# Performance work log

Measured on AMD Instinct MI355X. Metric: run time of the kernel, lower is better.

Reference implementation:

```python
import jax, jax.numpy as jnp
import numpy as np

B, N, K, NC, EMB, Z, AD = 16, 2048, 20, 16, 1024, 256, 64

def _lrelu(x):
    return jnp.where(x > 0, x, 0.2 * x)

def _bn(x, g, b, axes):
    # BatchNorm (training-mode batch stats, biased var, eps=1e-5); channel axis = 1
    m = x.mean(axes, keepdims=True)
    v = x.var(axes, keepdims=True)
    sh = [1] * x.ndim; sh[1] = -1
    return (x - m) * jax.lax.rsqrt(v + 1e-5) * g.reshape(sh) + b.reshape(sh)

def _c2(w, x):  # 1x1 Conv2d, no bias
    return jnp.einsum('oc,bcnk->bonk', w, x)

def _c1(w, x):  # 1x1 Conv1d, no bias
    return jnp.einsum('oc,bcn->bon', w, x)

def _knn(x, k):  # x: (B,C,N) -> idx (B,N,k)
    inner = -2.0 * jnp.einsum('bcn,bcm->bnm', x, x)
    xx = jnp.sum(x * x, axis=1)  # (B,N)
    pd = -xx[:, :, None] - inner - xx[:, None, :]  # negative squared dist
    return jax.lax.top_k(pd, k)[1]

def _graph_feat(x, idx):  # x: (B,C,N), idx: (B,N,k) -> (B,2C,N,k)
    xt = x.transpose(0, 2, 1)  # (B,N,C)
    feat = jax.vmap(lambda a, i: a[i])(xt, idx)  # (B,N,k,C)
    xc = jnp.broadcast_to(xt[:, :, None, :], feat.shape)
    return jnp.concatenate([feat - xc, xc], axis=-1).transpose(0, 3, 1, 2)

def setup_inputs():
    key = jax.random.key(0)
    ks = jax.random.split(key, 16)
    rn = lambda k, sh: (jax.random.normal(k, sh) * 0.05).astype(jnp.float32)
    d = {
        'xyz': jax.random.normal(ks[0], (B, N, 3), jnp.float32),
        'flow': jax.random.normal(ks[1], (B, N, 3), jnp.float32),
        'eps': jax.random.normal(ks[2], (B, Z), jnp.float32),
        'w_c1a': rn(ks[3], (60, 6)),   'w_c1b': rn(ks[4], (60, 60)),
        'w_c2a': rn(ks[5], (60, 120)), 'w_c2b': rn(ks[6], (60, 60)),
        'w_c3': rn(ks[7], (EMB, 120)),
        'w_mu': rn(ks[8], (Z, EMB)),  'b_mu': jnp.zeros((Z,), jnp.float32),
        'w_var': rn(ks[9], (Z, EMB)), 'b_var': jnp.zeros((Z,), jnp.float32),
        'w_enc': rn(ks[10], (64, NC)),
        'w_cub1': rn(ks[11], (256, Z + 64)), 'w_cub2': rn(ks[12], (120, 256)),
        'w_q': rn(ks[13], (AD, 120)), 'w_k': rn(ks[14], (AD, 120)),
    }
    for nm, c in [('c1a', 60), ('c1b', 60), ('c2a', 60), ('c2b', 60), ('c3', EMB)]:
        d['g_' + nm] = jnp.ones((c,), jnp.float32)
        d['bb_' + nm] = jnp.zeros((c,), jnp.float32)
    return d

def reference(xyz, flow, eps, w_c1a, w_c1b, w_c2a, w_c2b, w_c3, w_mu, b_mu,
              w_var, b_var, w_enc, w_cub1, w_cub2, w_q, w_k,
              g_c1a, bb_c1a, g_c1b, bb_c1b, g_c2a, bb_c2a, g_c2b, bb_c2b, g_c3, bb_c3):
    x = xyz.transpose(0, 2, 1)  # (B,3,N)
    idx = _knn(x, K)
    h = _graph_feat(x, idx)  # (B,6,N,K)
    h = _lrelu(_bn(_c2(w_c1a, h), g_c1a, bb_c1a, (0, 2, 3)))
    h = _lrelu(_bn(_c2(w_c1b, h), g_c1b, bb_c1b, (0, 2, 3)))
    x1 = h.max(axis=-1)  # (B,60,N)
    h = _graph_feat(x1, idx)  # low_dim_idx=1: reuse xyz knn
    h = _lrelu(_bn(_c2(w_c2a, h), g_c2a, bb_c2a, (0, 2, 3)))
    h = _lrelu(_bn(_c2(w_c2b, h), g_c2b, bb_c2b, (0, 2, 3)))
    x2 = h.max(axis=-1)
    x_per = jnp.concatenate([x1, x2], axis=1)  # (B,120,N)
    g = _lrelu(_bn(_c1(w_c3, x_per), g_c3, bb_c3, (0, 2))).max(axis=-1)  # (B,EMB)
    mu = g @ w_mu.T + b_mu
    log_var = g @ w_var.T + b_var
    z = eps * jnp.exp(0.5 * log_var) + mu  # (B,Z)
    cub = jnp.broadcast_to(jnp.eye(NC, dtype=xyz.dtype), (xyz.shape[0], NC, NC))
    cvec = _lrelu(_c1(w_enc, cub))  # (B,64,NC)
    xc = jnp.concatenate([jnp.broadcast_to(z[:, :, None], (z.shape[0], Z, NC)), cvec], axis=1)
    xc = _lrelu(_c1(w_cub1, xc))
    x_cuboid = _lrelu(_c1(w_cub2, xc))  # (B,120,NC)
    Q = _c1(w_q, x_per) / jnp.sqrt(jnp.float32(AD))  # (B,AD,N)
    Kf = _c1(w_k, x_cuboid)  # (B,AD,NC)
    scores = jnp.einsum('bcm,bcn->bmn', Kf, Q)  # (B,NC,N)
    assign = jax.nn.softmax(scores, axis=1).transpose(0, 2, 1)  # (B,N,NC)
    return (x_per, x_cuboid, z[:, :, None], mu, log_var, assign)
```

## Files before the change

kernel.cpp:

```cpp
#include <hip/hip_runtime.h>

typedef unsigned int u32;
typedef unsigned short u16;

#define BB 16
#define NN 2048
#define KK 20
#define EE (BB*NN*KK)
#define PP (BB*NN)
#define NCHK 8
#define CHKSZ (NN/NCHK)

#define O_XPER 0
#define O_XCUB 3932160
#define O_Z    3962880
#define O_MU   3966976
#define O_LV   3971072
#define O_ASG  3975168

__device__ double g_part[524288];
__device__ double g_std[2560];
__device__ float  g_st[2560];
__device__ float  g_zf[BB*256];
__device__ float  g_Kf[BB*1024];
__device__ u16    g_idx[EE];
__device__ float  g_xpf[(size_t)PP*120];
__device__ float  g_e1[(size_t)EE*60];
__device__ float  g_e2[(size_t)EE*60];

#define S1B_D 128
#define S2A_D 256
#define S2B_D 384
#define S1A_AB 0
#define S1B_AB 128
#define S2A_AB 256
#define S2B_AB 384
#define S3A 512
#define S3B 1536

#define MB_OFF 320000

#define NEG_BIG -1.0e30f

__device__ __forceinline__ float lrelu(float x){ return x > 0.f ? x : 0.2f*x; }

__device__ __forceinline__ void xrow(int bn, int c0, int cnt, float* d){
  const float* s = g_xpf + (size_t)bn*120 + c0;
  #pragma unroll 4
  for (int i=0;i<cnt;i+=4){
    float4 v = *(const float4*)(s+i);
    d[i]=v.x; d[i+1]=v.y; d[i+2]=v.z; d[i+3]=v.w;
  }
}

__device__ __forceinline__ float pdcalc(float4 pm, float qx, float qy, float qz, float qw){
  float dot = fmaf(qx,pm.x, fmaf(qy,pm.y, qz*pm.z));
  float t = fmaf(2.f, dot, -qw);
  return t - pm.w;
}

#define KT_DECL \
  float td0=NEG_BIG,td1=NEG_BIG,td2=NEG_BIG,td3=NEG_BIG,td4=NEG_BIG, \
        td5=NEG_BIG,td6=NEG_BIG,td7=NEG_BIG,td8=NEG_BIG,td9=NEG_BIG, \
        td10=NEG_BIG,td11=NEG_BIG,td12=NEG_BIG,td13=NEG_BIG,td14=NEG_BIG, \
        td15=NEG_BIG,td16=NEG_BIG,td17=NEG_BIG,td18=NEG_BIG,td19=NEG_BIG;
#define KT_CSW(u,l) { float mx = fmaxf(td##u, td##l); float mn = fminf(td##u, td##l); td##u = mx; td##l = mn; }
#define KT_INSERT(pd) \
  if ((pd) > td19){ \
    td19 = (pd); \
    KT_CSW(18,19) KT_CSW(17,18) KT_CSW(16,17) KT_CSW(15,16) \
    KT_CSW(14,15) KT_CSW(13,14) KT_CSW(12,13) KT_CSW(11,12) \
    KT_CSW(10,11) KT_CSW(9,10)  KT_CSW(8,9)   KT_CSW(7,8)   \
    KT_CSW(6,7)   KT_CSW(5,6)   KT_CSW(4,5)   KT_CSW(3,4)   \
    KT_CSW(2,3)   KT_CSW(1,2)   KT_CSW(0,1) }

__global__ __launch_bounds__(128) void k_knnt(const float* __restrict__ xyz){
  __shared__ float4 cand[CHKSZ];
  int qg = blockIdx.x >> 3;
  int c  = blockIdx.x & 7;
  int b  = qg >> 4;
  int n0 = (qg & 15) << 7;
  int t  = threadIdx.x;
  int m0 = c*CHKSZ;
  for (int i=t;i<CHKSZ;i+=128){
    const float* s = xyz + ((size_t)((b<<11)+m0+i))*3;
    float x=s[0], y=s[1], z=s[2];
    cand[i] = make_float4(x,y,z, fmaf(x,x,fmaf(y,y,z*z)));
  }
  __syncthreads();
  int n = n0 + t;
  const float* qs = xyz + ((size_t)((b<<11)+n))*3;
  float qx=qs[0], qy=qs[1], qz=qs[2];
  float qw = fmaf(qx,qx,fmaf(qy,qy,qz*qz));
  KT_DECL
  for (int i=0;i<CHKSZ;i++){
    float pd = pdcalc(cand[i], qx,qy,qz,qw);
    KT_INSERT(pd)
  }
  int p = (b<<11) + n;
  float* outd = g_e1;
  #define KOUT(k) outd[(size_t)(c*KK+k)*PP + p] = td##k;
  KOUT(0) KOUT(1) KOUT(2) KOUT(3) KOUT(4) KOUT(5) KOUT(6) KOUT(7) KOUT(8) KOUT(9)
  KOUT(10) KOUT(11) KOUT(12) KOUT(13) KOUT(14) KOUT(15) KOUT(16) KOUT(17) KOUT(18) KOUT(19)
  #undef KOUT
}

__global__ __launch_bounds__(256) void k_knnu(){
  int q = blockIdx.x*256 + threadIdx.x;
  const float* ind = g_e1;
  KT_DECL
  for (int i=0;i<NCHK*KK;i++){
    float pd = ind[(size_t)i*PP + q];
    KT_INSERT(pd)
  }
  g_e2[q] = td19;
}

__global__ __launch_bounds__(256) void k_knns1(const float* __restrict__ xyz){
  __shared__ float4 cand[CHKSZ];
  int gid = blockIdx.x*256 + threadIdx.x;
  int c = gid >> 15;
  int q = gid & (PP-1);
  int b = q >> 11;
  int t = threadIdx.x;
  for (int i=t;i<CHKSZ;i+=256){
    const float* s = xyz + ((size_t)((b<<11)+c*CHKSZ+i))*3;
    float x=s[0], y=s[1], z=s[2];
    cand[i] = make_float4(x,y,z, fmaf(x,x,fmaf(y,y,z*z)));
  }
  __syncthreads();
  const float* qs = xyz + (size_t)q*3;
  float qx=qs[0], qy=qs[1], qz=qs[2];
  float qw = fmaf(qx,qx,fmaf(qy,qy,qz*qz));
  float T = g_e2[q];
  u32 cgt=0, ceq=0;
  for (int i=0;i<CHKSZ;i++){
    float pd = pdcalc(cand[i], qx,qy,qz,qw);
    cgt += (pd > T) ? 1u : 0u;
    ceq += (pd == T) ? 1u : 0u;
  }
  u32* cntg = (u32*)g_part;
  u32* cnte = cntg + NCHK*PP;
  cntg[c*PP + q] = cgt;
  cnte[c*PP + q] = ceq;
}

__global__ __launch_bounds__(256) void k_knns2(){
  int q = blockIdx.x*256 + threadIdx.x;
  u32* cntg = (u32*)g_part;
  u32* cnte = cntg + NCHK*PP;
  u32* bg   = cnte + NCHK*PP;
  u32* be   = bg   + NCHK*PP;
  u32 acc = 0;
  for (int c=0;c<NCHK;c++){ bg[c*PP+q] = acc; acc += cntg[c*PP+q]; }
  u32 eacc = acc;
  for (int c=0;c<NCHK;c++){ be[c*PP+q] = eacc; eacc += cnte[c*PP+q]; }
}

__global__ __launch_bounds__(256) void k_knns3(const float* __restrict__ xyz){
  __shared__ float4 cand[CHKSZ];
  int gid = blockIdx.x*256 + threadIdx.x;
  int c = gid >> 15;
  int q = gid & (PP-1);
  int b = q >> 11;
  int t = threadIdx.x;
  for (int i=t;i<CHKSZ;i+=256){
    const float* s = xyz + ((size_t)((b<<11)+c*CHKSZ+i))*3;
    float x=s[0], y=s[1], z=s[2];
    cand[i] = make_float4(x,y,z, fmaf(x,x,fmaf(y,y,z*z)));
  }
  __syncthreads();
  const float* qs = xyz + (size_t)q*3;
  float qx=qs[0], qy=qs[1], qz=qs[2];
  float qw = fmaf(qx,qx,fmaf(qy,qy,qz*qz));
  float T = g_e2[q];
  const u32* cntg = (const u32*)g_part;
  const u32* cnte = cntg + NCHK*PP;
  const u32* bg   = cnte + NCHK*PP;
  const u32* be   = bg   + NCHK*PP;
  u32 wgt = bg[c*PP+q];
  u32 weq = be[c*PP+q];
  u16* o = g_idx + (size_t)q*KK;
  for (int i=0;i<CHKSZ;i++){
    float pd = pdcalc(cand[i], qx,qy,qz,qw);
    int m = c*CHKSZ + i;
    if (pd > T && wgt < KK){ o[wgt] = (u16)m; wgt++; }
    else if (pd == T && weq < KK){ o[weq] = (u16)m; weq++; }
  }
}

__global__ __launch_bounds__(256) void k_red60(int dbase, int nblk){
  __shared__ double red[256];
  int s = blockIdx.x;
  int t = threadIdx.x;
  double acc = 0.0;
  for (int i=t;i<nblk;i+=256) acc += g_part[(size_t)i*128 + s];
  red[t] = acc; __syncthreads();
  for (int w=128; w>0; w>>=1){ if (t<w) red[t]+=red[t+w]; __syncthreads(); }
  if (t==0) g_std[dbase+s] = red[0];
}

__global__ __launch_bounds__(64) void k_fin(const float* __restrict__ g, const float* __restrict__ bb,
                                            int dbase, int abase, double invc){
  int c = threadIdx.x;
  if (c < 60){
    double m = g_std[dbase+c]*invc;
    double v = g_std[dbase+64+c]*invc - m*m;
    if (v < 0.0) v = 0.0;
    float r = (float)(1.0/sqrt(v + 1e-5));
    float a = r*g[c];
    g_st[abase+c] = a;
    g_st[abase+64+c] = bb[c] - (float)m*a;
  }
}

__global__ __launch_bounds__(256) void k_gram1(const float* __restrict__ xyz){
  __shared__ double sred[128];
  int tid = threadIdx.x, lane = tid & 63, wv = tid >> 6;
  double acc[27];
  #pragma unroll
  for (int k=0;k<27;k++) acc[k]=0.0;
  for (int it=0; it<8; ++it){
    int edge = (it*320 + blockIdx.x)*256 + tid;
    int row = edge / KK;
    int b = row >> 11;
    int nbr = g_idx[edge];
    const float* cp = xyz + (size_t)row*3;
    const float* np2 = xyz + ((size_t)((b<<11)+nbr))*3;
    float f3=cp[0], f4=cp[1], f5=cp[2];
    float f0=np2[0]-f3, f1=np2[1]-f4, f2=np2[2]-f5;
    float f[6] = {f0,f1,f2,f3,f4,f5};
    #pragma unroll
    for (int i=0;i<6;i++) acc[i] += (double)f[i];
    int k=6;
    #pragma unroll
    for (int i=0;i<6;i++)
      #pragma unroll
      for (int j=i;j<6;j++){ acc[k] += (double)f[i]*(double)f[j]; k++; }
  }
  #pragma unroll
  for (int k=0;k<27;k++){
    double s = acc[k];
    #pragma unroll
    for (int m=1;m<64;m<<=1) s += __shfl_xor(s,m);
    if (lane==0) sred[wv*32+k] = s;
  }
  __syncthreads();
  if (tid < 27)
    g_part[(size_t)blockIdx.x*32 + tid] = sred[tid] + sred[32+tid] + sred[64+tid] + sred[96+tid];
}

__global__ __launch_bounds__(64) void k_fing1(const float* __restrict__ w1a,
                                              const float* __restrict__ gg, const float* __restrict__ bb){
  __shared__ double gsum[27];
  int t = threadIdx.x;
  if (t < 27){
    double s = 0.0;
    for (int i=0;i<320;i++) s += g_part[(size_t)i*32 + t];
    gsum[t] = s;
  }
  __syncthreads();
  if (t < 60){
    float w[6];
    #pragma unroll
    for (int i=0;i<6;i++) w[i] = w1a[t*6+i];
    double S = 0.0;
    #pragma unroll
    for (int i=0;i<6;i++) S += (double)w[i]*gsum[i];
    double Q = 0.0; int k = 6;
    #pragma unroll
    for (int i=0;i<6;i++)
      #pragma unroll
      for (int j=i;j<6;j++){
        double cf = (i==j) ? 1.0 : 2.0;
        Q += cf*(double)w[i]*(double)w[j]*gsum[k]; k++;
      }
    double inv1 = 1.0/(double)EE;
    double m = S*inv1;
    double v = Q*inv1 - m*m;
    if (v < 0.0) v = 0.0;
    float r = (float)(1.0/sqrt(v + 1e-5));
    float A = r*gg[t];
    g_st[S1A_AB+t] = A;
    g_st[S1A_AB+64+t] = bb[t] - (float)m*A;
  }
}

__global__ __launch_bounds__(256) void k_conv1b(const float* __restrict__ xyz,
                                                const float* __restrict__ w1a, const float* __restrict__ w1b){
  __shared__ float ws[360];
  __shared__ float wbs[3600];
  __shared__ float As[60], Bs[60];
  __shared__ double sred[512];
  int tid = threadIdx.x, lane = tid & 63, wv = tid >> 6;
  for (int i=tid;i<360;i+=256) ws[i]=w1a[i];
  for (int i=tid;i<3600;i+=256) wbs[i]=w1b[i];
  if (tid<60){ As[tid]=g_st[S1A_AB+tid]; Bs[tid]=g_st[S1A_AB+64+tid]; }
  __syncthreads();
  int edge = blockIdx.x*256 + tid;
  int row = edge / KK;
  int b = row >> 11;
  int nbr = g_idx[edge];
  const float* cp = xyz + (size_t)row*3;
  const float* np2 = xyz + ((size_t)((b<<11)+nbr))*3;
  float c0=cp[0], c1=cp[1], c2=cp[2];
  float d0=np2[0]-c0, d1=np2[1]-c1, d2=np2[2]-c2;
  float h[60];
  #pragma unroll 4
  for (int o=0;o<60;o++){
    float y = ws[o*6]*d0 + ws[o*6+1]*d1 + ws[o*6+2]*d2 + ws[o*6+3]*c0 + ws[o*6+4]*c1 + ws[o*6+5]*c2;
    h[o] = lrelu(fmaf(As[o], y, Bs[o]));
  }
  double rs=0.0, rq=0.0;
  for (int o=0;o<60;o++){
    float y=0.f;
    #pragma unroll
    for (int c=0;c<60;c++) y = fmaf(wbs[o*60+c], h[c], y);
    g_e2[(size_t)o*EE + edge] = y;
    float s=y, q=y*y;
    #pragma unroll
    for (int m=1;m<64;m<<=1){ s += __shfl_xor(s,m); q += __shfl_xor(q,m); }
    if (lane==o){ rs += (double)s; rq += (double)q; }
  }
  sred[wv*128 + lane] = rs;
  sred[wv*128 + 64 + lane] = rq;
  __syncthreads();
  if (tid < 128)
    g_part[(size_t)blockIdx.x*128 + tid] = sred[tid] + sred[128+tid] + sred[256+tid] + sred[384+tid];
}

__global__ __launch_bounds__(256) void k_final1s(float* __restrict__ outb){
  int o = blockIdx.x >> 7;
  int bn = ((blockIdx.x & 127) << 8) + threadIdx.x;
  int b = bn >> 11, n = bn & 2047;
  float A = g_st[S1B_AB+o], Bv = g_st[S1B_AB+64+o];
  const float* src = g_e2 + (size_t)o*EE + (size_t)bn*KK;
  float mx = NEG_BIG;
  #pragma unroll
  for (int k=0;k<KK;k++) mx = fmaxf(mx, lrelu(fmaf(A, src[k], Bv)));
  g_xpf[(size_t)bn*120 + o] = mx;
  outb[O_XPER + (size_t)(b*120+o)*NN + n] = mx;
}

__global__ __launch_bounds__(256) void k_pgem2(const float* __restrict__ w2a){
  __shared__ float wd[3600], wcd[3600];
  int tid = threadIdx.x;
  for (int i=tid;i<3600;i+=256){
    int o = i/60, c = i%60;
    float a = w2a[o*120+c], bvl = w2a[o*120+60+c];
    wd[i] = a; wcd[i] = bvl - a;
  }
  __syncthreads();
  int p = blockIdx.x*256 + tid;
  float x[60];
  xrow(p, 0, 60, x);
  float* gU = g_e2;
  float* gV = g_e2 + (size_t)PP*64;
  #pragma unroll 4
  for (int o=0;o<60;o++){
    float u=0.f, v=0.f;
    #pragma unroll
    for (int c=0;c<60;c++){ u = fmaf(wd[o*60+c], x[c], u); v = fmaf(wcd[o*60+c], x[c], v); }
    gU[(size_t)p*64 + o] = u;
    gV[(size_t)p*64 + o] = v;
  }
}

__global__ __launch_bounds__(256) void k_conv2a(){
  __shared__ double sred[512];
  int tid = threadIdx.x, lane = tid & 63, wv = tid >> 6;
  int edge = blockIdx.x*256 + tid;
  int row = edge / KK;
  int b = row >> 11;
  int nbr = g_idx[edge];
  int pn = (b<<11)+nbr;
  const float4* gU = (const float4*)g_e2;
  const float4* gV = (const float4*)(g_e2 + (size_t)PP*64);
  double rs=0.0, rq=0.0;
  #pragma unroll
  for (int o4=0;o4<15;o4++){
    float4 uu = gU[(size_t)pn*16 + o4];
    float4 vv = gV[(size_t)row*16 + o4];
    float y0=uu.x+vv.x, y1=uu.y+vv.y, y2=uu.z+vv.z, y3=uu.w+vv.w;
    g_e1[(size_t)(o4*4+0)*EE + edge] = y0;
    g_e1[(size_t)(o4*4+1)*EE + edge] = y1;
    g_e1[(size_t)(o4*4+2)*EE + edge] = y2;
    g_e1[(size_t)(o4*4+3)*EE + edge] = y3;
    float ys[4] = {y0,y1,y2,y3};
    #pragma unroll
    for (int j=0;j<4;j++){
      float s=ys[j], q=ys[j]*ys[j];
      #pragma unroll
      for (int m=1;m<64;m<<=1){ s += __shfl_xor(s,m); q += __shfl_xor(q,m); }
      if (lane==o4*4+j){ rs += (double)s; rq += (double)q; }
    }
  }
  sred[wv*128 + lane] = rs;
  sred[wv*128 + 64 + lane] = rq;
  __syncthreads();
  if (tid < 128)
    g_part[(size_t)blockIdx.x*128 + tid] = sred[tid] + sred[128+tid] + sred[256+tid] + sred[384+tid];
}

__global__ __launch_bounds__(256) void k_conv2b(const float* __restrict__ w2b){
  __shared__ float wbs[3600];
  __shared__ float As[60], Bs[60];
  __shared__ double sred[512];
  int tid = threadIdx.x, lane = tid & 63, wv = tid >> 6;
  for (int i=tid;i<3600;i+=256) wbs[i]=w2b[i];
  if (tid<60){ As[tid]=g_st[S2A_AB+tid]; Bs[tid]=g_st[S2A_AB+64+tid]; }
  __syncthreads();
  int edge = blockIdx.x*256 + tid;
  float h[60];
  #pragma unroll 4
  for (int o=0;o<60;o++) h[o] = lrelu(fmaf(As[o], g_e1[(size_t)o*EE + edge], Bs[o]));
  double rs=0.0, rq=0.0;
  for (int o=0;o<60;o++){
    float y=0.f;
    #pragma unroll
    for (int c=0;c<60;c++) y = fmaf(wbs[o*60+c], h[c], y);
    g_e2[(size_t)o*EE + edge] = y;
    float s=y, q=y*y;
    #pragma unroll
    for (int m=1;m<64;m<<=1){ s += __shfl_xor(s,m); q += __shfl_xor(q,m); }
    if (lane==o){ rs += (double)s; rq += (double)q; }
  }
  sred[wv*128 + lane] = rs;
  sred[wv*128 + 64 + lane] = rq;
  __syncthreads();
  if (tid < 128)
    g_part[(size_t)blockIdx.x*128 + tid] = sred[tid] + sred[128+tid] + sred[256+tid] + sred[384+tid];
}

__global__ __launch_bounds__(256) void k_final2s(float* __restrict__ outb){
  int o = blockIdx.x >> 7;
  int bn = ((blockIdx.x & 127) << 8) + threadIdx.x;
  int b = bn >> 11, n = bn & 2047;
  float A = g_st[S2B_AB+o], Bv = g_st[S2B_AB+64+o];
  const float* src = g_e2 + (size_t)o*EE + (size_t)bn*KK;
  float mx = NEG_BIG;
  #pragma unroll
  for (int k=0;k<KK;k++) mx = fmaxf(mx, lrelu(fmaf(A, src[k], Bv)));
  g_xpf[(size_t)bn*120 + 60 + o] = mx;
  outb[O_XPER + (size_t)(b*120+60+o)*NN + n] = mx;
}

__global__ __launch_bounds__(256) void k_max3s2(const float* __restrict__ wc3){
  __shared__ float xt[64*120];
  __shared__ float redA[256], redB[256], redS[256], redQ[256];
  int tid = threadIdx.x;
  int pj = tid>>6, ei = tid&63;
  int ec = blockIdx.x>>6;
  int b  = (blockIdx.x>>2)&15;
  int seg= blockIdx.x&3;
  int e  = ec*64 + ei;
  float w[120];
  {
    const float4* wp = (const float4*)(wc3 + (size_t)e*120);
    #pragma unroll
    for (int c4=0;c4<30;c4++){
      float4 t = wp[c4];
      w[c4*4]=t.x; w[c4*4+1]=t.y; w[c4*4+2]=t.z; w[c4*4+3]=t.w;
    }
  }
  float mx = NEG_BIG, mn = -NEG_BIG, S = 0.f, Q = 0.f;
  for (int tile=0; tile<8; tile++){
    int p0 = b*2048 + seg*512 + tile*64;
    __syncthreads();
    for (int v=tid; v<1920; v+=256){
      int pk = v/30, c4 = v%30;
      ((float4*)xt)[pk*30+c4] = *(const float4*)(g_xpf + (size_t)(p0+pk)*120 + c4*4);
    }
    __syncthreads();
    for (int k=pj*16; k<pj*16+16; k++){
      const float* xr = xt + k*120;
      float a0=0.f,a1=0.f,a2=0.f,a3=0.f;
      #pragma unroll
      for (int c=0;c<120;c+=4){
        a0 = fmaf(w[c],   xr[c],   a0);
        a1 = fmaf(w[c+1], xr[c+1], a1);
        a2 = fmaf(w[c+2], xr[c+2], a2);
        a3 = fmaf(w[c+3], xr[c+3], a3);
      }
      float y = (a0+a1)+(a2+a3);
      mx = fmaxf(mx, y);
      mn = fminf(mn, y);
      S += y;
      Q = fmaf(y, y, Q);
    }
  }
  __syncthreads();
  redA[tid]=mx; redB[tid]=mn; redS[tid]=S; redQ[tid]=Q;
  __syncthreads();
  if (pj==0){
    float M  = fmaxf(fmaxf(redA[ei],redA[64+ei]), fmaxf(redA[128+ei],redA[192+ei]));
    float m2 = fminf(fminf(redB[ei],redB[64+ei]), fminf(redB[128+ei],redB[192+ei]));
    float Ss = (redS[ei]+redS[64+ei])+(redS[128+ei]+redS[192+ei]);
    float Qs = (redQ[ei]+redQ[64+ei])+(redQ[128+ei]+redQ[192+ei]);
    float* MB = (float*)(g_part + MB_OFF);
    int slot = (seg*16+b)*1024 + e;
    MB[slot]          = M;
    MB[65536  + slot] = m2;
    MB[131072 + slot] = Ss;
    MB[196608 + slot] = Qs;
  }
}

__global__ __launch_bounds__(64) void k_fin3R(const float* __restrict__ gg, const float* __restrict__ bb){
  int e = blockIdx.x*64 + threadIdx.x;
  const float* MB = (const float*)(g_part + MB_OFF);
  double S=0.0, Q=0.0;
  for (int j=0;j<64;j++){
    S += (double)MB[131072 + j*1024 + e];
    Q += (double)MB[196608 + j*1024 + e];
  }
  double inv3 = 1.0/(double)PP;
  double m = S*inv3;
  double v = Q*inv3 - m*m;
  if (v < 0.0) v = 0.0;
  float r = (float)(1.0/sqrt(v + 1e-5));
  float A = r*gg[e];
  g_st[S3A+e] = A;
  g_st[S3B+e] = bb[e] - (float)m*A;
}

__global__ __launch_bounds__(256) void k_head(const float* __restrict__ eps,
                                              const float* __restrict__ wmu, const float* __restrict__ bmu,
                                              const float* __restrict__ wvar, const float* __restrict__ bvar,
                                              float* __restrict__ outb){
  int b = blockIdx.x, j = threadIdx.x;
  __shared__ float gs[1024];
  const float* MB = (const float*)(g_part + MB_OFF);
  for (int i=j;i<1024;i+=256){
    float A = g_st[S3A+i], B = g_st[S3B+i];
    float M = NEG_BIG, m2 = -NEG_BIG;
    #pragma unroll
    for (int sg=0;sg<4;sg++){
      M  = fmaxf(M,  MB[(sg*16+b)*1024 + i]);
      m2 = fminf(m2, MB[65536 + (sg*16+b)*1024 + i]);
    }
    float y = (A > 0.f) ? M : ((A < 0.f) ? m2 : M);
    gs[i] = lrelu(fmaf(A, y, B));
  }
  __syncthreads();
  float mu = bmu[j], lv = bvar[j];
  const float4* wm = (const float4*)(wmu + (size_t)j*1024);
  const float4* wv = (const float4*)(wvar + (size_t)j*1024);
  #pragma unroll 4
  for (int e=0;e<256;e++){
    float4 a = wm[e], c = wv[e];
    const float* g4 = gs + e*4;
    mu = fmaf(a.x,g4[0], fmaf(a.y,g4[1], fmaf(a.z,g4[2], fmaf(a.w,g4[3], mu))));
    lv = fmaf(c.x,g4[0], fmaf(c.y,g4[1], fmaf(c.z,g4[2], fmaf(c.w,g4[3], lv))));
  }
  float z = fmaf(eps[b*256+j], expf(0.5f*lv), mu);
  g_zf[b*256+j] = z;
  outb[O_MU + b*256 + j] = mu;
  outb[O_LV + b*256 + j] = lv;
  outb[O_Z  + b*256 + j] = z;
}

__global__ __launch_bounds__(256) void k_cuboid(const float* __restrict__ wenc,
                                                const float* __restrict__ wcub1, const float* __restrict__ wcub2,
                                                const float* __restrict__ wk, float* __restrict__ outb){
  int b = blockIdx.x, t = threadIdx.x;
  __shared__ float xc[320*16];
  __shared__ float hh[256*16];
  __shared__ float xq[120*16];
  for (int i=t;i<320*16;i+=256){
    int c = i>>4, m = i&15;
    xc[i] = (c<256) ? g_zf[b*256+c] : lrelu(wenc[(c-256)*16+m]);
  }
  __syncthreads();
  {
    float acc[16];
    #pragma unroll
    for (int m=0;m<16;m++) acc[m]=0.f;
    for (int c=0;c<320;c++){
      float wv = wcub1[(size_t)t*320+c];
      #pragma unroll
      for (int m=0;m<16;m++) acc[m] = fmaf(wv, xc[c*16+m], acc[m]);
    }
    #pragma unroll
    for (int m=0;m<16;m++) hh[t*16+m] = lrelu(acc[m]);
  }
  __syncthreads();
  if (t<120){
    float a2[16];
    #pragma unroll
    for (int m=0;m<16;m++) a2[m]=0.f;
    for (int c=0;c<256;c++){
      float wv = wcub2[(size_t)t*256+c];
      #pragma unroll
      for (int m=0;m<16;m++) a2[m] = fmaf(wv, hh[c*16+m], a2[m]);
    }
    #pragma unroll
    for (int m=0;m<16;m++){
      float v = lrelu(a2[m]);
      xq[t*16+m] = v;
      outb[O_XCUB + b*1920 + t*16 + m] = v;
    }
  }
  __syncthreads();
  if (t<64){
    float a3[16];
    #pragma unroll
    for (int m=0;m<16;m++) a3[m]=0.f;
    for (int c=0;c<120;c++){
      float wv = wk[t*120+c];
      #pragma unroll
      for (int m=0;m<16;m++) a3[m] = fmaf(wv, xq[c*16+m], a3[m]);
    }
    #pragma unroll
    for (int m=0;m<16;m++) g_Kf[b*1024 + t*16 + m] = a3[m];
  }
}

__global__ __launch_bounds__(64) void k_attn(const float* __restrict__ wq, float* __restrict__ outb){
  int p = blockIdx.x*64 + threadIdx.x;
  int b = p >> 11;
  float x[120];
  xrow(p, 0, 120, x);
  float sc[16];
  #pragma unroll
  for (int m=0;m<16;m++) sc[m]=0.f;
  for (int a=0;a<64;a++){
    float q=0.f;
    #pragma unroll
    for (int c=0;c<120;c++) q = fmaf(wq[a*120+c], x[c], q);
    q *= 0.125f;
    const float* kf = g_Kf + b*1024 + a*16;
    #pragma unroll
    for (int m=0;m<16;m++) sc[m] = fmaf(kf[m], q, sc[m]);
  }
  float mx = sc[0];
  #pragma unroll
  for (int m=1;m<16;m++) mx = fmaxf(mx, sc[m]);
  float s=0.f;
  #pragma unroll
  for (int m=0;m<16;m++){ sc[m] = expf(sc[m]-mx); s += sc[m]; }
  float inv = 1.f/s;
  #pragma unroll
  for (int m=0;m<16;m++) outb[O_ASG + (size_t)p*16 + m] = sc[m]*inv;
}

extern "C" void kernel_launch(void* const* d_in, const int* in_sizes, int n_in,
                              void* d_out, int out_size, void* d_ws, size_t ws_size,
                              hipStream_t stream){
  const float* xyz  = (const float*)d_in[0];
  const float* eps  = (const float*)d_in[2];
  const float* w1a  = (const float*)d_in[3];
  const float* w1b  = (const float*)d_in[4];
  const float* w2a  = (const float*)d_in[5];
  const float* w2b  = (const float*)d_in[6];
  const float* wc3  = (const float*)d_in[7];
  const float* wmu  = (const float*)d_in[8];
  const float* bmu  = (const float*)d_in[9];
  const float* wvar = (const float*)d_in[10];
  const float* bvar = (const float*)d_in[11];
  const float* wenc = (const float*)d_in[12];
  const float* wcub1= (const float*)d_in[13];
  const float* wcub2= (const float*)d_in[14];
  const float* wq   = (const float*)d_in[15];
  const float* wk   = (const float*)d_in[16];
  const float* g1a  = (const float*)d_in[17];
  const float* b1a  = (const float*)d_in[18];
  const float* g1b  = (const float*)d_in[19];
  const float* b1b  = (const float*)d_in[20];
  const float* g2a  = (const float*)d_in[21];
  const float* b2a  = (const float*)d_in[22];
  const float* g2b  = (const float*)d_in[23];
  const float* b2b  = (const float*)d_in[24];
  const float* g3   = (const float*)d_in[25];
  const float* b3   = (const float*)d_in[26];
  float* outb = (float*)d_out;

  const double inv1 = 1.0/(double)EE;

  k_knnt<<<2048,128,0,stream>>>(xyz);
  k_knnu<<<128,256,0,stream>>>();
  k_knns1<<<1024,256,0,stream>>>(xyz);
  k_knns2<<<128,256,0,stream>>>();
  k_knns3<<<1024,256,0,stream>>>(xyz);
  k_gram1<<<320,256,0,stream>>>(xyz);
  k_fing1<<<1,64,0,stream>>>(w1a, g1a, b1a);
  k_conv1b<<<2560,256,0,stream>>>(xyz, w1a, w1b);
  k_red60<<<128,256,0,stream>>>(S1B_D, 2560);
  k_fin<<<1,64,0,stream>>>(g1b, b1b, S1B_D, S1B_AB, inv1);
  k_final1s<<<7680,256,0,stream>>>(outb);
  k_pgem2<<<128,256,0,stream>>>(w2a);
  k_conv2a<<<2560,256,0,stream>>>();
  k_red60<<<128,256,0,stream>>>(S2A_D, 2560);
  k_fin<<<1,64,0,stream>>>(g2a, b2a, S2A_D, S2A_AB, inv1);
  k_conv2b<<<2560,256,0,stream>>>(w2b);
  k_red60<<<128,256,0,stream>>>(S2B_D, 2560);
  k_fin<<<1,64,0,stream>>>(g2b, b2b, S2B_D, S2B_AB, inv1);
  k_final2s<<<7680,256,0,stream>>>(outb);
  k_max3s2<<<1024,256,0,stream>>>(wc3);
  k_fin3R<<<16,64,0,stream>>>(g3, b3);
  k_head<<<16,256,0,stream>>>(eps, wmu, bmu, wvar, bvar, outb);
  k_cuboid<<<16,256,0,stream>>>(wenc, wcub1, wcub2, wk, outb);
  k_attn<<<512,64,0,stream>>>(wq, outb);
}
```

Before: 1.320 ms.

## Restructure conv3 max/stat kernel to per-thread channels with broadcast global loads

Replaces the shared-memory tiled conv3 kernel with one in which each thread owns one output channel and streams 256 points straight from global memory as float4 loads. Every lane in a block reads the same address, so the loads are broadcasts. This removes the LDS staging, the block barriers and the cross-warp reduction. The partial max/min/sum/sumsq buffers move into the g_e1 scratch array with 8 segments instead of 4, and the finalize and head kernels are updated to match. The trade-off is that it relies on cache broadcast for the x rows and launches half as many blocks, which gives less parallelism.

```diff
diff --git a/kernel.cpp b/kernel.cpp
--- a/kernel.cpp
+++ b/kernel.cpp
@@ -38,7 +38,10 @@
 #define S3A 512
 #define S3B 1536
 
-#define MB_OFF 320000
+#define P3_MX 0
+#define P3_MN 131072
+#define P3_S  262144
+#define P3_Q  393216
 
 #define NEG_BIG -1.0e30f
 
@@ -445,15 +448,12 @@
   outb[O_XPER + (size_t)(b*120+60+o)*NN + n] = mx;
 }
 
-__global__ __launch_bounds__(256) void k_max3s2(const float* __restrict__ wc3){
-  __shared__ float xt[64*120];
-  __shared__ float redA[256], redB[256], redS[256], redQ[256];
+__global__ __launch_bounds__(256) void k_max3s3(const float* __restrict__ wc3){
   int tid = threadIdx.x;
-  int pj = tid>>6, ei = tid&63;
-  int ec = blockIdx.x>>6;
-  int b  = (blockIdx.x>>2)&15;
-  int seg= blockIdx.x&3;
-  int e  = ec*64 + ei;
+  int ec  = blockIdx.x & 3;
+  int b   = (blockIdx.x >> 2) & 15;
+  int seg = blockIdx.x >> 6;
+  int e   = ec*256 + tid;
   float w[120];
   {
     const float4* wp = (const float4*)(wc3 + (size_t)e*120);
@@ -464,55 +464,37 @@
     }
   }
   float mx = NEG_BIG, mn = -NEG_BIG, S = 0.f, Q = 0.f;
-  for (int tile=0; tile<8; tile++){
-    int p0 = b*2048 + seg*512 + tile*64;
-    __syncthreads();
-    for (int v=tid; v<1920; v+=256){
-      int pk = v/30, c4 = v%30;
-      ((float4*)xt)[pk*30+c4] = *(const float4*)(g_xpf + (size_t)(p0+pk)*120 + c4*4);
-    }
-    __syncthreads();
-    for (int k=pj*16; k<pj*16+16; k++){
-      const float* xr = xt + k*120;
-      float a0=0.f,a1=0.f,a2=0.f,a3=0.f;
-      #pragma unroll
-      for (int c=0;c<120;c+=4){
-        a0 = fmaf(w[c],   xr[c],   a0);
-        a1 = fmaf(w[c+1], xr[c+1], a1);
-        a2 = fmaf(w[c+2], xr[c+2], a2);
-        a3 = fmaf(w[c+3], xr[c+3], a3);
-      }
-      float y = (a0+a1)+(a2+a3);
-      mx = fmaxf(mx, y);
-      mn = fminf(mn, y);
-      S += y;
-      Q = fmaf(y, y, Q);
-    }
-  }
-  __syncthreads();
-  redA[tid]=mx; redB[tid]=mn; redS[tid]=S; redQ[tid]=Q;
-  __syncthreads();
-  if (pj==0){
-    float M  = fmaxf(fmaxf(redA[ei],redA[64+ei]), fmaxf(redA[128+ei],redA[192+ei]));
-    float m2 = fminf(fminf(redB[ei],redB[64+ei]), fminf(redB[128+ei],redB[192+ei]));
-    float Ss = (redS[ei]+redS[64+ei])+(redS[128+ei]+redS[192+ei]);
-    float Qs = (redQ[ei]+redQ[64+ei])+(redQ[128+ei]+redQ[192+ei]);
-    float* MB = (float*)(g_part + MB_OFF);
-    int slot = (seg*16+b)*1024 + e;
-    MB[slot]          = M;
-    MB[65536  + slot] = m2;
-    MB[131072 + slot] = Ss;
-    MB[196608 + slot] = Qs;
-  }
+  int p0 = b*2048 + seg*256;
+  for (int k=0;k<256;k++){
+    const float4* xr = (const float4*)(g_xpf + (size_t)(p0+k)*120);
+    float a0=0.f,a1=0.f,a2=0.f,a3=0.f;
+    #pragma unroll
+    for (int c4=0;c4<30;c4++){
+      float4 xv = xr[c4];
+      a0 = fmaf(w[c4*4],   xv.x, a0);
+      a1 = fmaf(w[c4*4+1], xv.y, a1);
+      a2 = fmaf(w[c4*4+2], xv.z, a2);
+      a3 = fmaf(w[c4*4+3], xv.w, a3);
+    }
+    float y = (a0+a1)+(a2+a3);
+    mx = fmaxf(mx, y);
+    mn = fminf(mn, y);
+    S += y;
+    Q = fmaf(y, y, Q);
+  }
+  int slot = (seg*16+b)*1024 + e;
+  g_e1[P3_MX + slot] = mx;
+  g_e1[P3_MN + slot] = mn;
+  g_e1[P3_S  + slot] = S;
+  g_e1[P3_Q  + slot] = Q;
 }
 
 __global__ __launch_bounds__(64) void k_fin3R(const float* __restrict__ gg, const float* __restrict__ bb){
   int e = blockIdx.x*64 + threadIdx.x;
-  const float* MB = (const float*)(g_part + MB_OFF);
   double S=0.0, Q=0.0;
-  for (int j=0;j<64;j++){
-    S += (double)MB[131072 + j*1024 + e];
-    Q += (double)MB[196608 + j*1024 + e];
+  for (int j=0;j<128;j++){
+    S += (double)g_e1[P3_S + j*1024 + e];
+    Q += (double)g_e1[P3_Q + j*1024 + e];
   }
   double inv3 = 1.0/(double)PP;
   double m = S*inv3;
@@ -530,14 +512,13 @@
                                               float* __restrict__ outb){
   int b = blockIdx.x, j = threadIdx.x;
   __shared__ float gs[1024];
-  const float* MB = (const float*)(g_part + MB_OFF);
   for (int i=j;i<1024;i+=256){
     float A = g_st[S3A+i], B = g_st[S3B+i];
     float M = NEG_BIG, m2 = -NEG_BIG;
     #pragma unroll
-    for (int sg=0;sg<4;sg++){
-      M  = fmaxf(M,  MB[(sg*16+b)*1024 + i]);
-      m2 = fminf(m2, MB[65536 + (sg*16+b)*1024 + i]);
+    for (int sg=0;sg<8;sg++){
+      M  = fmaxf(M,  g_e1[P3_MX + (sg*16+b)*1024 + i]);
+      m2 = fminf(m2, g_e1[P3_MN + (sg*16+b)*1024 + i]);
     }
     float y = (A > 0.f) ? M : ((A < 0.f) ? m2 : M);
     gs[i] = lrelu(fmaf(A, y, B));
@@ -696,7 +677,7 @@
   k_red60<<<128,256,0,stream>>>(S2B_D, 2560);
   k_fin<<<1,64,0,stream>>>(g2b, b2b, S2B_D, S2B_AB, inv1);
   k_final2s<<<7680,256,0,stream>>>(outb);
-  k_max3s2<<<1024,256,0,stream>>>(wc3);
+  k_max3s3<<<512,256,0,stream>>>(wc3);
   k_fin3R<<<16,64,0,stream>>>(g3, b3);
   k_head<<<16,256,0,stream>>>(eps, wmu, bmu, wvar, bvar, outb);
   k_cuboid<<<16,256,0,stream>>>(wenc, wcub1, wcub2, wk, outb);
```

Measured after the change: 1.435 ms. 8.7% more time.
